# Kernel optimization log

Hardware: AMD Instinct MI355X
Metric: run time of the kernel (lower is better)

The kernel has to match this reference:

```python
import jax, jax.numpy as jnp
import numpy as np

C = 512
H = 8  # num_heads
GROUPS = 32
EPS = 1e-5


def group_norm(x, scale, bias):
    # x: [b, c, h, w]; GroupNorm(32, c) normalizes over (c//32, h, w) per group
    b, c, h, w = x.shape
    xg = x.reshape(b, GROUPS, c // GROUPS * h * w)
    mean = jnp.mean(xg, axis=-1, keepdims=True)
    var = jnp.var(xg, axis=-1, keepdims=True)
    xg = (xg - mean) * jax.lax.rsqrt(var + EPS)
    x = xg.reshape(b, c, h, w)
    return x * scale[None, :, None, None] + bias[None, :, None, None]


def setup_inputs() -> dict:
    key = jax.random.key(0)
    ks = jax.random.split(key, 6)
    init = 0.02
    return {
        "x": jax.random.normal(ks[0], (8, C, 32, 32), dtype=jnp.float32),
        "gn_scale": jnp.ones((C,), jnp.float32),
        "gn_bias": jnp.zeros((C,), jnp.float32),
        "Wq": jax.random.normal(ks[1], (C, C), jnp.float32) * init,
        "bq": jnp.zeros((C,), jnp.float32),
        "Wk": jax.random.normal(ks[2], (C, C), jnp.float32) * init,
        "bk": jnp.zeros((C,), jnp.float32),
        "Wv": jax.random.normal(ks[3], (C, C), jnp.float32) * init,
        "bv": jnp.zeros((C,), jnp.float32),
        "Wo": jax.random.normal(ks[4], (C, C), jnp.float32) * init,
        "bo": jnp.zeros((C,), jnp.float32),
    }


def reference(x, gn_scale, gn_bias, Wq, bq, Wk, bk, Wv, bv, Wo, bo):
    b, c, h, w = x.shape
    s = h * w  # number of spatial tokens
    d = c // H  # head dim
    residual = x
    xn = group_norm(x, gn_scale, gn_bias)
    t = xn.reshape(b, c, s).transpose(0, 2, 1)  # [b, s, c]
    # torch Linear: y = x @ W.T + b
    q = t @ Wq.T + bq
    k = t @ Wk.T + bk
    v = t @ Wv.T + bv
    q = q.reshape(b, s, H, d).transpose(0, 2, 1, 3)  # [b, H, s, d]
    k = k.reshape(b, s, H, d).transpose(0, 2, 1, 3)
    v = v.reshape(b, s, H, d).transpose(0, 2, 1, 3)
    scale = d ** -0.5
    attn = jnp.einsum('bhqd,bhkd->bhqk', q, k) * scale  # [b, H, s, s]
    attn = jax.nn.softmax(attn, axis=-1)
    out = jnp.einsum('bhqk,bhkd->bhqd', attn, v)  # [b, H, s, d]
    out = out.transpose(0, 2, 1, 3).reshape(b, s, c)
    out = out @ Wo.T + bo
    out = out.transpose(0, 2, 1).reshape(b, c, h, w)
    return out + residual
```

## Files before the change

### kernel.cpp

```cpp
#include <hip/hip_runtime.h>


typedef __bf16 bf16x8 __attribute__((ext_vector_type(8)));
typedef __bf16 bf16x4 __attribute__((ext_vector_type(4)));
typedef float floatx4 __attribute__((ext_vector_type(4)));

static __device__ __forceinline__ floatx4 mfma16(bf16x8 a, bf16x8 b, floatx4 c) {
  return __builtin_amdgcn_mfma_f32_16x16x32_bf16(a, b, c, 0, 0, 0);
}

static __device__ __forceinline__ void async_cp16(const void* g, void* l) {
  __builtin_amdgcn_global_load_lds(
      (const __attribute__((address_space(1))) unsigned int*)g,
      (__attribute__((address_space(3))) unsigned int*)l, 16, 0, 0);
}

__global__ __launch_bounds__(256) void prep_gn_kernel(
    const float* __restrict__ x, const float* __restrict__ gamma,
    const float* __restrict__ beta,
    const float* __restrict__ Wq, const float* __restrict__ bq,
    const float* __restrict__ Wk, const float* __restrict__ bk,
    const float* __restrict__ Wv, const float* __restrict__ bv,
    const float* __restrict__ Wo,
    __bf16* __restrict__ wqkv, __bf16* __restrict__ wo,
    float* __restrict__ bqkv, __bf16* __restrict__ t) {
  __shared__ __bf16 tile[16 * 1024];
  __shared__ float rbuf[8];
  int tid = threadIdx.x;
  int bx = blockIdx.x;

  if (bx >= 256) {
    const float SC = 0.125f * 1.4426950408889634f;
    int i = ((bx - 256) * 256 + tid) * 4;
    float4 q4 = *(const float4*)(Wq + i);
    float4 k4 = *(const float4*)(Wk + i);
    float4 v4 = *(const float4*)(Wv + i);
    float4 o4 = *(const float4*)(Wo + i);
    *(bf16x4*)(wqkv + i) = (bf16x4){(__bf16)(q4.x * SC), (__bf16)(q4.y * SC),
                                    (__bf16)(q4.z * SC), (__bf16)(q4.w * SC)};
    *(bf16x4*)(wqkv + 262144 + i) =
        (bf16x4){(__bf16)k4.x, (__bf16)k4.y, (__bf16)k4.z, (__bf16)k4.w};
    *(bf16x4*)(wqkv + 524288 + i) =
        (bf16x4){(__bf16)v4.x, (__bf16)v4.y, (__bf16)v4.z, (__bf16)v4.w};
    *(bf16x4*)(wo + i) =
        (bf16x4){(__bf16)o4.x, (__bf16)o4.y, (__bf16)o4.z, (__bf16)o4.w};
    int j = (bx - 256) * 256 + tid;
    if (j < 512) {
      bqkv[j]        = bq[j] * SC;
      bqkv[512 + j]  = bk[j];
      bqkv[1024 + j] = bv[j];
    }
    return;
  }

  int b = bx >> 5, g = bx & 31;
  const float* xp = x + (size_t)(b * 512 + g * 16) * 1024;
  const float4* xp4 = (const float4*)xp;

  float sacc = 0.f, ssacc = 0.f;
#pragma unroll
  for (int it = 0; it < 16; ++it) {
    float4 v = xp4[it * 256 + tid];
    sacc += v.x + v.y + v.z + v.w;
    ssacc += v.x * v.x + v.y * v.y + v.z * v.z + v.w * v.w;
  }
#pragma unroll
  for (int off = 1; off < 64; off <<= 1) {
    sacc += __shfl_xor(sacc, off);
    ssacc += __shfl_xor(ssacc, off);
  }
  int wv = tid >> 6;
  if ((tid & 63) == 0) { rbuf[wv] = sacc; rbuf[4 + wv] = ssacc; }
  __syncthreads();
  float S1 = rbuf[0] + rbuf[1] + rbuf[2] + rbuf[3];
  float S2 = rbuf[4] + rbuf[5] + rbuf[6] + rbuf[7];
  float mean = S1 * (1.f / 16384.f);
  float var = S2 * (1.f / 16384.f) - mean * mean;
  float inv = rsqrtf(var + 1e-5f);

#pragma unroll
  for (int it = 0; it < 16; ++it) {
    float4 v = xp4[it * 256 + tid];
    float ga = gamma[g * 16 + it], be = beta[g * 16 + it];
    int base = it * 1024 + tid * 4;
    tile[base + 0] = (__bf16)((v.x - mean) * inv * ga + be);
    tile[base + 1] = (__bf16)((v.y - mean) * inv * ga + be);
    tile[base + 2] = (__bf16)((v.z - mean) * inv * ga + be);
    tile[base + 3] = (__bf16)((v.w - mean) * inv * ga + be);
  }
  __syncthreads();

#pragma unroll
  for (int j = 0; j < 8; ++j) {
    int qid = j * 256 + tid;
    int sidx = qid >> 1, half = qid & 1;
    union { uint4 u; __bf16 h[8]; } o;
#pragma unroll
    for (int i = 0; i < 8; ++i) o.h[i] = tile[(half * 8 + i) * 1024 + sidx];
    *(uint4*)(t + (size_t)(b * 1024 + sidx) * 512 + g * 16 + half * 8) = o.u;
  }
}

__global__ __launch_bounds__(256) void gemm_qkv_kernel(
    const __bf16* __restrict__ t, const __bf16* __restrict__ wqkv,
    const float* __restrict__ bqkv,
    __bf16* __restrict__ qb, __bf16* __restrict__ kb, __bf16* __restrict__ vt) {
  __shared__ __align__(16) __bf16 smem[8192];
  __bf16* As = smem;
  __bf16* Bs = smem + 4096;
  int tid = threadIdx.x;
  int m0 = blockIdx.x * 128;
  int n0 = blockIdx.y * 128;
  int wave = tid >> 6, lane = tid & 63;
  int l15 = lane & 15, quad = lane >> 4;
  int wm = wave >> 1, wn = wave & 1;

  floatx4 acc[4][4];
#pragma unroll
  for (int mi = 0; mi < 4; ++mi)
#pragma unroll
    for (int ni = 0; ni < 4; ++ni) acc[mi][ni] = (floatx4){0.f, 0.f, 0.f, 0.f};

  int r1 = tid >> 2, o1 = (tid & 3) * 8;
  const __bf16* gA1 = t + (size_t)(m0 + r1) * 512 + o1;
  const __bf16* gA2 = t + (size_t)(m0 + 64 + r1) * 512 + o1;
  const __bf16* gB1 = wqkv + (size_t)(n0 + r1) * 512 + o1;
  const __bf16* gB2 = wqkv + (size_t)(n0 + 64 + r1) * 512 + o1;
  __bf16* lA1 = As + tid * 8;
  __bf16* lA2 = As + 2048 + tid * 8;
  __bf16* lB1 = Bs + tid * 8;
  __bf16* lB2 = Bs + 2048 + tid * 8;

  for (int k0 = 0; k0 < 512; k0 += 32) {
    async_cp16(gA1 + k0, lA1);
    async_cp16(gA2 + k0, lA2);
    async_cp16(gB1 + k0, lB1);
    async_cp16(gB2 + k0, lB2);
    __syncthreads();
    bf16x8 af[4], bfr[4];
#pragma unroll
    for (int mi = 0; mi < 4; ++mi)
      af[mi] = *(const bf16x8*)&As[(wm * 64 + mi * 16 + l15) * 32 + quad * 8];
#pragma unroll
    for (int ni = 0; ni < 4; ++ni)
      bfr[ni] = *(const bf16x8*)&Bs[(wn * 64 + ni * 16 + l15) * 32 + quad * 8];
#pragma unroll
    for (int mi = 0; mi < 4; ++mi)
#pragma unroll
      for (int ni = 0; ni < 4; ++ni)
        acc[mi][ni] = mfma16(af[mi], bfr[ni], acc[mi][ni]);
    __syncthreads();
  }

  int mat = n0 >> 9;
  int bidx = m0 >> 10, s0 = m0 & 1023;
  int hA = (n0 & 511) >> 6;
  float bias[4];
#pragma unroll
  for (int ni = 0; ni < 4; ++ni)
    bias[ni] = bqkv[n0 + wn * 64 + ni * 16 + l15];

  if (mat < 2) {
    __bf16* dst = (mat == 0) ? qb : kb;
    for (int c = 0; c < 4; ++c) {
      if ((c >> 1) == wm) {
#pragma unroll
        for (int mi2 = 0; mi2 < 2; ++mi2) {
          int mi = (c & 1) * 2 + mi2;
          int lrow = mi2 * 16 + quad * 4;
#pragma unroll
          for (int ni = 0; ni < 4; ++ni)
#pragma unroll
            for (int r = 0; r < 4; ++r)
              smem[(lrow + r) * 136 + wn * 64 + ni * 16 + l15] =
                  (__bf16)(acc[mi][ni][r] + bias[ni]);
        }
      }
      __syncthreads();
#pragma unroll
      for (int u = 0; u < 2; ++u) {
        int f = tid * 16 + u * 8;
        int row = f >> 7, col = f & 127;
        uint4 val = *(uint4*)&smem[row * 136 + col];
        int head = hA + (col >> 6), d = col & 63;
        *(uint4*)(dst + ((size_t)(bidx * 8 + head) * 1024 + s0 + c * 32 + row) * 64 + d) = val;
      }
      __syncthreads();
    }
  } else {
    for (int c = 0; c < 4; ++c) {
      if ((c >> 1) == wn) {
#pragma unroll
        for (int ni2 = 0; ni2 < 2; ++ni2) {
          int ni = (c & 1) * 2 + ni2;
          int nrow = ni2 * 16 + l15;
#pragma unroll
          for (int mi = 0; mi < 4; ++mi)
#pragma unroll
            for (int r = 0; r < 4; ++r)
              smem[nrow * 136 + wm * 64 + mi * 16 + quad * 4 + r] =
                  (__bf16)(acc[mi][ni][r] + bias[ni]);
        }
      }
      __syncthreads();
#pragma unroll
      for (int u = 0; u < 2; ++u) {
        int f = tid * 16 + u * 8;
        int nrow = f >> 7, mcol = f & 127;
        uint4 val = *(uint4*)&smem[nrow * 136 + mcol];
        int nloc = c * 32 + nrow;
        int head = hA + (nloc >> 6), d = nloc & 63;
        *(uint4*)(vt + ((size_t)(bidx * 8 + head) * 64 + d) * 1024 + s0 + mcol) = val;
      }
      __syncthreads();
    }
  }
}

__global__ __launch_bounds__(256) void attn_kernel(
    const __bf16* __restrict__ qb, const __bf16* __restrict__ kb,
    const __bf16* __restrict__ vt, __bf16* __restrict__ ao) {
  __shared__ __align__(16) __bf16 Ks[2][64 * 72];
  __shared__ __align__(16) __bf16 Vs[2][64 * 72];
  __shared__ __align__(16) __bf16 Ps[128 * 72];
  int tid = threadIdx.x;
  int bx = blockIdx.x;
  int b = bx >> 6, h = (bx >> 3) & 7, q128 = bx & 7;
  int wv = tid >> 6, lane = tid & 63, l15 = lane & 15, quad = lane >> 4;
  size_t bh = (size_t)(b * 8 + h) * 65536;
  const __bf16* Qp = qb + bh;
  const __bf16* Kp = kb + bh;
  const __bf16* Vp = vt + bh;
  int q0 = q128 * 128, qw = q0 + wv * 32;

  bf16x8 aq[2][2];
#pragma unroll
  for (int mi = 0; mi < 2; ++mi)
#pragma unroll
    for (int kh = 0; kh < 2; ++kh)
      aq[mi][kh] = *(const bf16x8*)(Qp + (size_t)(qw + mi * 16 + l15) * 64 + kh * 32 + quad * 8);

  bf16x8 ones;
#pragma unroll
  for (int i = 0; i < 8; ++i) ones[i] = (__bf16)1.0f;

  floatx4 oacc[2][4], lacc[2];
#pragma unroll
  for (int mi = 0; mi < 2; ++mi) {
    lacc[mi] = (floatx4){0.f, 0.f, 0.f, 0.f};
#pragma unroll
    for (int di = 0; di < 4; ++di) oacc[mi][di] = (floatx4){0.f, 0.f, 0.f, 0.f};
  }

  int srow = tid >> 3, scol = (tid & 7) * 8;
  int ldsoff = srow * 72 + scol;

  uint4 kr0, kr1, vr0, vr1;
  kr0 = *(const uint4*)(Kp + (size_t)srow * 64 + scol);
  kr1 = *(const uint4*)(Kp + (size_t)(srow + 32) * 64 + scol);
  vr0 = *(const uint4*)(Vp + (size_t)srow * 1024 + scol);
  vr1 = *(const uint4*)(Vp + (size_t)(srow + 32) * 1024 + scol);

  for (int kt = 0; kt < 16; ++kt) {
    int cur = kt & 1;
    *(uint4*)&Ks[cur][ldsoff] = kr0;
    *(uint4*)&Ks[cur][ldsoff + 32 * 72] = kr1;
    *(uint4*)&Vs[cur][ldsoff] = vr0;
    *(uint4*)&Vs[cur][ldsoff + 32 * 72] = vr1;
    if (kt < 15) {
      int nt = kt + 1;
      kr0 = *(const uint4*)(Kp + (size_t)(nt * 64 + srow) * 64 + scol);
      kr1 = *(const uint4*)(Kp + (size_t)(nt * 64 + srow + 32) * 64 + scol);
      vr0 = *(const uint4*)(Vp + (size_t)srow * 1024 + nt * 64 + scol);
      vr1 = *(const uint4*)(Vp + (size_t)(srow + 32) * 1024 + nt * 64 + scol);
    }
    __syncthreads();

    floatx4 sa[2][4];
#pragma unroll
    for (int ni = 0; ni < 4; ++ni) {
      bf16x8 bk0 = *(const bf16x8*)&Ks[cur][(ni * 16 + l15) * 72 + quad * 8];
      bf16x8 bk1 = *(const bf16x8*)&Ks[cur][(ni * 16 + l15) * 72 + 32 + quad * 8];
#pragma unroll
      for (int mi = 0; mi < 2; ++mi) {
        floatx4 s4 = (floatx4){0.f, 0.f, 0.f, 0.f};
        s4 = mfma16(aq[mi][0], bk0, s4);
        s4 = mfma16(aq[mi][1], bk1, s4);
        sa[mi][ni] = s4;
      }
    }

#pragma unroll
    for (int mi = 0; mi < 2; ++mi)
#pragma unroll
      for (int ni = 0; ni < 4; ++ni)
#pragma unroll
        for (int r = 0; r < 4; ++r)
          Ps[(wv * 32 + mi * 16 + quad * 4 + r) * 72 + ni * 16 + l15] =
              (__bf16)__builtin_amdgcn_exp2f(sa[mi][ni][r]);

#pragma unroll
    for (int mi = 0; mi < 2; ++mi) {
      bf16x8 ap0 = *(const bf16x8*)&Ps[(wv * 32 + mi * 16 + l15) * 72 + quad * 8];
      bf16x8 ap1 = *(const bf16x8*)&Ps[(wv * 32 + mi * 16 + l15) * 72 + 32 + quad * 8];
#pragma unroll
      for (int di = 0; di < 4; ++di) {
        bf16x8 bv0 = *(const bf16x8*)&Vs[cur][(di * 16 + l15) * 72 + quad * 8];
        bf16x8 bv1 = *(const bf16x8*)&Vs[cur][(di * 16 + l15) * 72 + 32 + quad * 8];
        oacc[mi][di] = mfma16(ap0, bv0, oacc[mi][di]);
        oacc[mi][di] = mfma16(ap1, bv1, oacc[mi][di]);
      }
      lacc[mi] = mfma16(ap0, ones, lacc[mi]);
      lacc[mi] = mfma16(ap1, ones, lacc[mi]);
    }
  }

#pragma unroll
  for (int mi = 0; mi < 2; ++mi)
#pragma unroll
    for (int r = 0; r < 4; ++r) {
      float invl = 1.f / lacc[mi][r];
      int lrow = wv * 32 + mi * 16 + quad * 4 + r;
#pragma unroll
      for (int di = 0; di < 4; ++di)
        Ps[lrow * 72 + di * 16 + l15] = (__bf16)(oacc[mi][di][r] * invl);
    }
  __syncthreads();
  __bf16* aop = ao + (size_t)b * 524288 + h * 64;
#pragma unroll
  for (int u = 0; u < 4; ++u) {
    int idx = u * 256 + tid;
    int row = idx >> 3, col = (idx & 7) * 8;
    *(uint4*)(aop + (size_t)(q0 + row) * 512 + col) = *(uint4*)&Ps[row * 72 + col];
  }
}

__global__ __launch_bounds__(256) void gemm_out_kernel(
    const __bf16* __restrict__ ao, const __bf16* __restrict__ wo,
    const float* __restrict__ bo, const float* __restrict__ x,
    float* __restrict__ out) {
  __shared__ __align__(16) __bf16 As[128 * 32];
  __shared__ __align__(16) __bf16 Bs[128 * 32];
  __shared__ __align__(16) float ctile[32 * 132];
  int tid = threadIdx.x;
  int m0 = blockIdx.x * 128;
  int n0 = blockIdx.y * 128;
  int wave = tid >> 6, lane = tid & 63;
  int l15 = lane & 15, quad = lane >> 4;
  int wm = wave >> 1, wn = wave & 1;

  floatx4 acc[4][4];
#pragma unroll
  for (int mi = 0; mi < 4; ++mi)
#pragma unroll
    for (int ni = 0; ni < 4; ++ni) acc[mi][ni] = (floatx4){0.f, 0.f, 0.f, 0.f};

  int r1 = tid >> 2, o1 = (tid & 3) * 8;
  const __bf16* gA1 = ao + (size_t)(m0 + r1) * 512 + o1;
  const __bf16* gA2 = ao + (size_t)(m0 + 64 + r1) * 512 + o1;
  const __bf16* gB1 = wo + (size_t)(n0 + r1) * 512 + o1;
  const __bf16* gB2 = wo + (size_t)(n0 + 64 + r1) * 512 + o1;
  __bf16* lA1 = As + tid * 8;
  __bf16* lA2 = As + 2048 + tid * 8;
  __bf16* lB1 = Bs + tid * 8;
  __bf16* lB2 = Bs + 2048 + tid * 8;

  for (int k0 = 0; k0 < 512; k0 += 32) {
    async_cp16(gA1 + k0, lA1);
    async_cp16(gA2 + k0, lA2);
    async_cp16(gB1 + k0, lB1);
    async_cp16(gB2 + k0, lB2);
    __syncthreads();
    bf16x8 af[4], bfr[4];
#pragma unroll
    for (int mi = 0; mi < 4; ++mi)
      af[mi] = *(const bf16x8*)&As[(wm * 64 + mi * 16 + l15) * 32 + quad * 8];
#pragma unroll
    for (int ni = 0; ni < 4; ++ni)
      bfr[ni] = *(const bf16x8*)&Bs[(wn * 64 + ni * 16 + l15) * 32 + quad * 8];
#pragma unroll
    for (int mi = 0; mi < 4; ++mi)
#pragma unroll
      for (int ni = 0; ni < 4; ++ni)
        acc[mi][ni] = mfma16(af[mi], bfr[ni], acc[mi][ni]);
    __syncthreads();
  }

  int b = m0 >> 10, s0 = m0 & 1023;
  for (int cc = 0; cc < 4; ++cc) {
    __syncthreads();
    if (wn == (cc >> 1)) {
#pragma unroll
      for (int nis = 0; nis < 2; ++nis) {
        int ni = (cc & 1) * 2 + nis;
        int nn = nis * 16 + l15;
        int n = n0 + wn * 64 + ni * 16 + l15;
        float bias = bo[n];
#pragma unroll
        for (int mi = 0; mi < 4; ++mi)
#pragma unroll
          for (int r = 0; r < 4; ++r)
            ctile[nn * 132 + wm * 64 + mi * 16 + quad * 4 + r] =
                acc[mi][ni][r] + bias;
      }
    }
    __syncthreads();
    int nn = tid >> 3, mlb = (tid & 7) * 16;
    int n = n0 + cc * 32 + nn;
    const float* xr = x + (size_t)(b * 512 + n) * 1024 + s0;
    float* orow = out + (size_t)(b * 512 + n) * 1024 + s0;
#pragma unroll
    for (int i = 0; i < 16; i += 4) {
      float4 cv = *(float4*)&ctile[nn * 132 + mlb + i];
      float4 xv = *(const float4*)&xr[mlb + i];
      float4 ov = {cv.x + xv.x, cv.y + xv.y, cv.z + xv.z, cv.w + xv.w};
      *(float4*)&orow[mlb + i] = ov;
    }
  }
}

extern "C" void kernel_launch(void* const* d_in, const int* in_sizes, int n_in,
                              void* d_out, int out_size, void* d_ws, size_t ws_size,
                              hipStream_t stream) {
  const float* x  = (const float*)d_in[0];
  const float* gs = (const float*)d_in[1];
  const float* gb = (const float*)d_in[2];
  const float* Wq = (const float*)d_in[3];
  const float* bq = (const float*)d_in[4];
  const float* Wk = (const float*)d_in[5];
  const float* bk = (const float*)d_in[6];
  const float* Wv = (const float*)d_in[7];
  const float* bv = (const float*)d_in[8];
  const float* Wo = (const float*)d_in[9];
  const float* bo = (const float*)d_in[10];
  float* out = (float*)d_out;

  char* ws = (char*)d_ws;
  __bf16* wqkv = (__bf16*)(ws);
  __bf16* wo   = (__bf16*)(ws + 1572864);
  float*  bqkv = (float*)(ws + 2097152);
  __bf16* t    = (__bf16*)(ws + 2103296);
  __bf16* ao   = t;
  __bf16* qb   = (__bf16*)(ws + 10491904);
  __bf16* kb   = (__bf16*)(ws + 18880512);
  __bf16* vtb  = (__bf16*)(ws + 27269120);

  prep_gn_kernel<<<dim3(512), dim3(256), 0, stream>>>(
      x, gs, gb, Wq, bq, Wk, bk, Wv, bv, Wo, wqkv, wo, bqkv, t);
  gemm_qkv_kernel<<<dim3(64, 12), dim3(256), 0, stream>>>(t, wqkv, bqkv, qb, kb, vtb);
  attn_kernel<<<dim3(512), dim3(256), 0, stream>>>(qb, kb, vtb, ao);
  gemm_out_kernel<<<dim3(64, 4), dim3(256), 0, stream>>>(ao, wo, bo, x, out);
}
```

Baseline: 164.9 us.

## Transpose QK MFMA output for packed P stores; halve out-GEMM N tile

In the attention kernel, the QK^T MFMA operands are swapped so each lane holds four consecutive key columns of a row. The exp'd probabilities can then be written to LDS as one packed bf16x4 store instead of four scalar stores. The PV loop is reordered to load each V fragment once and reuse it across both row blocks. The output projection GEMM tile shrinks from 128x128 to 128x64 and the grid doubles to 512 blocks, trading more A-tile reloads for better CU occupancy and fill across the GPU.

```diff
diff --git a/kernel.cpp b/kernel.cpp
--- a/kernel.cpp
+++ b/kernel.cpp
@@ -284,8 +284,8 @@
 #pragma unroll
       for (int mi = 0; mi < 2; ++mi) {
         floatx4 s4 = (floatx4){0.f, 0.f, 0.f, 0.f};
-        s4 = mfma16(aq[mi][0], bk0, s4);
-        s4 = mfma16(aq[mi][1], bk1, s4);
+        s4 = mfma16(bk0, aq[mi][0], s4);
+        s4 = mfma16(bk1, aq[mi][1], s4);
         sa[mi][ni] = s4;
       }
     }
@@ -293,25 +293,34 @@
 #pragma unroll
     for (int mi = 0; mi < 2; ++mi)
 #pragma unroll
-      for (int ni = 0; ni < 4; ++ni)
+      for (int ni = 0; ni < 4; ++ni) {
+        bf16x4 pk;
 #pragma unroll
         for (int r = 0; r < 4; ++r)
-          Ps[(wv * 32 + mi * 16 + quad * 4 + r) * 72 + ni * 16 + l15] =
-              (__bf16)__builtin_amdgcn_exp2f(sa[mi][ni][r]);
-
+          pk[r] = (__bf16)__builtin_amdgcn_exp2f(sa[mi][ni][r]);
+        *(bf16x4*)&Ps[(wv * 32 + mi * 16 + l15) * 72 + ni * 16 + quad * 4] = pk;
+      }
+
+    bf16x8 ap[2][2];
 #pragma unroll
     for (int mi = 0; mi < 2; ++mi) {
-      bf16x8 ap0 = *(const bf16x8*)&Ps[(wv * 32 + mi * 16 + l15) * 72 + quad * 8];
-      bf16x8 ap1 = *(const bf16x8*)&Ps[(wv * 32 + mi * 16 + l15) * 72 + 32 + quad * 8];
-#pragma unroll
-      for (int di = 0; di < 4; ++di) {
-        bf16x8 bv0 = *(const bf16x8*)&Vs[cur][(di * 16 + l15) * 72 + quad * 8];
-        bf16x8 bv1 = *(const bf16x8*)&Vs[cur][(di * 16 + l15) * 72 + 32 + quad * 8];
-        oacc[mi][di] = mfma16(ap0, bv0, oacc[mi][di]);
-        oacc[mi][di] = mfma16(ap1, bv1, oacc[mi][di]);
-      }
-      lacc[mi] = mfma16(ap0, ones, lacc[mi]);
-      lacc[mi] = mfma16(ap1, ones, lacc[mi]);
+      ap[mi][0] = *(const bf16x8*)&Ps[(wv * 32 + mi * 16 + l15) * 72 + quad * 8];
+      ap[mi][1] = *(const bf16x8*)&Ps[(wv * 32 + mi * 16 + l15) * 72 + 32 + quad * 8];
+    }
+#pragma unroll
+    for (int di = 0; di < 4; ++di) {
+      bf16x8 bv0 = *(const bf16x8*)&Vs[cur][(di * 16 + l15) * 72 + quad * 8];
+      bf16x8 bv1 = *(const bf16x8*)&Vs[cur][(di * 16 + l15) * 72 + 32 + quad * 8];
+#pragma unroll
+      for (int mi = 0; mi < 2; ++mi) {
+        oacc[mi][di] = mfma16(ap[mi][0], bv0, oacc[mi][di]);
+        oacc[mi][di] = mfma16(ap[mi][1], bv1, oacc[mi][di]);
+      }
+    }
+#pragma unroll
+    for (int mi = 0; mi < 2; ++mi) {
+      lacc[mi] = mfma16(ap[mi][0], ones, lacc[mi]);
+      lacc[mi] = mfma16(ap[mi][1], ones, lacc[mi]);
     }
   }
 
@@ -340,62 +349,57 @@
     const float* __restrict__ bo, const float* __restrict__ x,
     float* __restrict__ out) {
   __shared__ __align__(16) __bf16 As[128 * 32];
-  __shared__ __align__(16) __bf16 Bs[128 * 32];
+  __shared__ __align__(16) __bf16 Bs[64 * 32];
   __shared__ __align__(16) float ctile[32 * 132];
   int tid = threadIdx.x;
   int m0 = blockIdx.x * 128;
-  int n0 = blockIdx.y * 128;
+  int n0 = blockIdx.y * 64;
   int wave = tid >> 6, lane = tid & 63;
   int l15 = lane & 15, quad = lane >> 4;
   int wm = wave >> 1, wn = wave & 1;
 
-  floatx4 acc[4][4];
+  floatx4 acc[4][2];
 #pragma unroll
   for (int mi = 0; mi < 4; ++mi)
 #pragma unroll
-    for (int ni = 0; ni < 4; ++ni) acc[mi][ni] = (floatx4){0.f, 0.f, 0.f, 0.f};
+    for (int ni = 0; ni < 2; ++ni) acc[mi][ni] = (floatx4){0.f, 0.f, 0.f, 0.f};
 
   int r1 = tid >> 2, o1 = (tid & 3) * 8;
   const __bf16* gA1 = ao + (size_t)(m0 + r1) * 512 + o1;
   const __bf16* gA2 = ao + (size_t)(m0 + 64 + r1) * 512 + o1;
   const __bf16* gB1 = wo + (size_t)(n0 + r1) * 512 + o1;
-  const __bf16* gB2 = wo + (size_t)(n0 + 64 + r1) * 512 + o1;
   __bf16* lA1 = As + tid * 8;
   __bf16* lA2 = As + 2048 + tid * 8;
   __bf16* lB1 = Bs + tid * 8;
-  __bf16* lB2 = Bs + 2048 + tid * 8;
 
   for (int k0 = 0; k0 < 512; k0 += 32) {
     async_cp16(gA1 + k0, lA1);
     async_cp16(gA2 + k0, lA2);
     async_cp16(gB1 + k0, lB1);
-    async_cp16(gB2 + k0, lB2);
-    __syncthreads();
-    bf16x8 af[4], bfr[4];
+    __syncthreads();
+    bf16x8 af[4], bfr[2];
 #pragma unroll
     for (int mi = 0; mi < 4; ++mi)
       af[mi] = *(const bf16x8*)&As[(wm * 64 + mi * 16 + l15) * 32 + quad * 8];
 #pragma unroll
-    for (int ni = 0; ni < 4; ++ni)
-      bfr[ni] = *(const bf16x8*)&Bs[(wn * 64 + ni * 16 + l15) * 32 + quad * 8];
+    for (int ni = 0; ni < 2; ++ni)
+      bfr[ni] = *(const bf16x8*)&Bs[(wn * 32 + ni * 16 + l15) * 32 + quad * 8];
 #pragma unroll
     for (int mi = 0; mi < 4; ++mi)
 #pragma unroll
-      for (int ni = 0; ni < 4; ++ni)
+      for (int ni = 0; ni < 2; ++ni)
         acc[mi][ni] = mfma16(af[mi], bfr[ni], acc[mi][ni]);
     __syncthreads();
   }
 
   int b = m0 >> 10, s0 = m0 & 1023;
-  for (int cc = 0; cc < 4; ++cc) {
-    __syncthreads();
-    if (wn == (cc >> 1)) {
-#pragma unroll
-      for (int nis = 0; nis < 2; ++nis) {
-        int ni = (cc & 1) * 2 + nis;
-        int nn = nis * 16 + l15;
-        int n = n0 + wn * 64 + ni * 16 + l15;
-        float bias = bo[n];
+  for (int cc = 0; cc < 2; ++cc) {
+    __syncthreads();
+    if (wn == cc) {
+#pragma unroll
+      for (int ni = 0; ni < 2; ++ni) {
+        int nn = ni * 16 + l15;
+        float bias = bo[n0 + cc * 32 + nn];
 #pragma unroll
         for (int mi = 0; mi < 4; ++mi)
 #pragma unroll
@@ -449,5 +453,5 @@
       x, gs, gb, Wq, bq, Wk, bk, Wv, bv, Wo, wqkv, wo, bqkv, t);
   gemm_qkv_kernel<<<dim3(64, 12), dim3(256), 0, stream>>>(t, wqkv, bqkv, qb, kb, vtb);
   attn_kernel<<<dim3(512), dim3(256), 0, stream>>>(qb, kb, vtb, ao);
-  gemm_out_kernel<<<dim3(64, 4), dim3(256), 0, stream>>>(ao, wo, bo, x, out);
-}
+  gemm_out_kernel<<<dim3(64, 8), dim3(256), 0, stream>>>(ao, wo, bo, x, out);
+}
```

Result: faster. 157.6 us (-4.4%).
